# Kernel optimization log

Measured on AMD Instinct MI355X. Metric: run time of the kernel, lower is better.

Reference implementation:

```python
import jax, jax.numpy as jnp
import numpy as np

B, L, N_IN, NUM_CLASS = 2, 256, 128, 1
INIT_STD = 0.01


def setup_inputs() -> dict:
    key = jax.random.key(0)
    kx, ky, kz, kw = jax.random.split(key, 4)
    x = jax.random.normal(kx, (B, L, N_IN), dtype=jnp.float32)
    y = jax.random.normal(ky, (B, L, N_IN), dtype=jnp.float32)
    z = jax.random.normal(kz, (B, L, N_IN), dtype=jnp.float32)
    # weight: [n_in + bias_x, n_in, n_in + bias_y, num_class], init ~ N(0, init_std)
    weight = jax.random.normal(kw, (N_IN + 1, N_IN, N_IN + 1, NUM_CLASS), dtype=jnp.float32) * INIT_STD
    return {"x": x, "y": y, "z": z, "weight": weight}


def reference(x, y, z, weight):
    # bias_x / bias_y: append a ones column to x and y
    xb = jnp.concatenate([x, jnp.ones_like(x[..., :1])], axis=-1)  # [B, L, n_in+1]
    yb = jnp.concatenate([y, jnp.ones_like(y[..., :1])], axis=-1)  # [B, L, n_in+1]
    # 4-way triaffine contraction -> [B, Lx, Ly, Lz, r]
    s = jnp.einsum('bxi,bzk,ikjr,byj->bxyzr', xb, z, weight, yb, optimize=True)
    # num_class == 1: squeeze last dim (original returns before applying scale)
    return s[..., 0]
```

## Files before the change

### kernel.cpp

```cpp
#include <hip/hip_runtime.h>


typedef __bf16 bf16x8 __attribute__((ext_vector_type(8)));
typedef short short4_t __attribute__((ext_vector_type(4)));
typedef float f32x4 __attribute__((ext_vector_type(4)));
typedef unsigned short ushort4_t __attribute__((ext_vector_type(4)));

#define LL 256
#define NI 128
#define NFLATP 17408
#define KJ_STRIDE 136
#define XB_STRIDE 132
#define P_STRIDE 132

__device__ __forceinline__ unsigned short f2bf(float f) {
    unsigned u = __builtin_bit_cast(unsigned, f);
    u += 0x7FFFu + ((u >> 16) & 1u);
    return (unsigned short)(u >> 16);
}
__device__ __forceinline__ float bf2f(unsigned short h) {
    return __builtin_bit_cast(float, (unsigned)h << 16);
}

__global__ __launch_bounds__(512) void stage1f_kernel(const float* __restrict__ W,
                                                      const float* __restrict__ x,
                                                      const float* __restrict__ y,
                                                      const float* __restrict__ z,
                                                      unsigned short* __restrict__ yzbf,
                                                      unsigned short* __restrict__ A2g) {
    const int blk = blockIdx.x, tid = threadIdx.x;

    if (blk >= 272) {
        int t = (blk - 272) * 512 + tid;
        int base = t * 4;
        int which = base >> 16;
        int local = base & 65535;
        const float* s = which ? z : y;
        float4 v = *(const float4*)(s + local);
        ushort4_t o;
        o[0] = f2bf(v.x); o[1] = f2bf(v.y); o[2] = f2bf(v.z); o[3] = f2bf(v.w);
        *(ushort4_t*)(yzbf + base) = o;
        return;
    }

    const int bxg = blk & 1;
    const int nb  = blk >> 1;

    __shared__ unsigned short T[128 * KJ_STRIDE];
    __shared__ unsigned short XB[256 * XB_STRIDE];

    {
        const int nl = tid & 127;
        const int ig = tid >> 7;
        const int np = nb * 128 + nl;
        const int k  = np / KJ_STRIDE;
        const int j  = np - k * KJ_STRIDE;
        const bool jok = (j <= 128);
        const float* Wkj = W + (size_t)k * 129 + j;
        float wreg[33];
#pragma unroll
        for (int r = 0; r < 33; ++r) {
            int i = ig + r * 4;
            wreg[r] = (i <= 128 && jok) ? Wkj[(size_t)i * 16512] : 0.f;
        }
#pragma unroll
        for (int r = 0; r < 33; ++r) {
            int i = ig + r * 4;
            if (i <= 128) T[nl * KJ_STRIDE + i] = f2bf(wreg[r]);
        }
    }

    {
        const float* xsrc = x + (size_t)bxg * 256 * NI;
#pragma unroll 4
        for (int c = 0; c < 16; ++c) {
            int idx = c * 512 + tid;
            float4 v = *(const float4*)(xsrc + (size_t)idx * 4);
            int fid = idx * 4;
            int row = fid >> 7, col = fid & 127;
            ushort4_t o;
            o[0] = f2bf(v.x); o[1] = f2bf(v.y); o[2] = f2bf(v.z); o[3] = f2bf(v.w);
            *(ushort4_t*)&XB[row * XB_STRIDE + col] = o;
        }
    }
    __syncthreads();

    const int wv = tid >> 6, lane = tid & 63;
    const int l15 = lane & 15, h = lane >> 4;
    const int nsub = wv & 3;
    const int bxh  = wv >> 2;
    const int nloc = nsub * 32;
    const int nglob = nb * 128 + nloc;
    const int bx0 = bxg * 256 + bxh * 128;

    bf16x8 af[2][4];
#pragma unroll
    for (int nt = 0; nt < 2; ++nt)
#pragma unroll
        for (int is = 0; is < 4; ++is)
            af[nt][is] = *(const bf16x8*)&T[(nloc + nt * 16 + l15) * KJ_STRIDE + is * 32 + 8 * h];

    f32x4 acc[2][8];
#pragma unroll
    for (int nt = 0; nt < 2; ++nt) {
        f32x4 binit;
#pragma unroll
        for (int r = 0; r < 4; ++r)
            binit[r] = bf2f(T[(nloc + nt * 16 + 4 * h + r) * KJ_STRIDE + 128]);
#pragma unroll
        for (int ct = 0; ct < 8; ++ct) acc[nt][ct] = binit;
    }

#pragma unroll
    for (int is = 0; is < 4; ++is)
#pragma unroll
        for (int ct = 0; ct < 8; ++ct) {
            bf16x8 xf = *(const bf16x8*)&XB[(bxh * 128 + ct * 16 + l15) * XB_STRIDE + is * 32 + 8 * h];
            acc[0][ct] = __builtin_amdgcn_mfma_f32_16x16x32_bf16(af[0][is], xf, acc[0][ct], 0, 0, 0);
            acc[1][ct] = __builtin_amdgcn_mfma_f32_16x16x32_bf16(af[1][is], xf, acc[1][ct], 0, 0, 0);
        }

#pragma unroll
    for (int nt = 0; nt < 2; ++nt)
#pragma unroll
        for (int ct = 0; ct < 8; ++ct) {
            ushort4_t o;
#pragma unroll
            for (int r = 0; r < 4; ++r) o[r] = f2bf(acc[nt][ct][r]);
            *(ushort4_t*)(A2g + (size_t)(bx0 + ct * 16 + l15) * NFLATP + nglob + nt * 16 + 4 * h) = o;
        }
}

__global__ __launch_bounds__(512, 4) void stage2_kernel(const unsigned short* __restrict__ ybf,
                                                        const unsigned short* __restrict__ zbf,
                                                        const unsigned short* __restrict__ A2g,
                                                        float* __restrict__ out) {
    const int bx  = blockIdx.x;
    const int b   = bx >> 8;
    const int tid = threadIdx.x;
    const int wv = tid >> 6, lane = tid & 63;
    const int l15 = lane & 15, h = lane >> 4;

    __shared__ __align__(16) unsigned short SH[LL * P_STRIDE];

    {
        const float4* src = (const float4*)(A2g + (size_t)bx * NFLATP);
        float4* dst = (float4*)SH;
        for (int t = tid; t < NFLATP / 8; t += 512) dst[t] = src[t];
    }
    __syncthreads();

    const unsigned short* yb = ybf + b * LL * NI;
    const unsigned short* zb = zbf + b * LL * NI;
    const int y0 = wv * 32;

    f32x4 accP[8][2];
#pragma unroll
    for (int kt = 0; kt < 8; ++kt)
#pragma unroll
        for (int r = 0; r < 4; ++r) {
            float bias = bf2f(SH[(kt * 16 + 4 * h + r) * KJ_STRIDE + 128]);
            accP[kt][0][r] = bias; accP[kt][1][r] = bias;
        }
#pragma unroll
    for (int js = 0; js < 4; ++js) {
        bf16x8 yf[2];
#pragma unroll
        for (int yt = 0; yt < 2; ++yt)
            yf[yt] = *(const bf16x8*)(yb + (y0 + yt * 16 + l15) * NI + js * 32 + 8 * h);
#pragma unroll
        for (int kt = 0; kt < 8; ++kt) {
            bf16x8 af = *(const bf16x8*)&SH[(kt * 16 + l15) * KJ_STRIDE + js * 32 + 8 * h];
            accP[kt][0] = __builtin_amdgcn_mfma_f32_16x16x32_bf16(af, yf[0], accP[kt][0], 0, 0, 0);
            accP[kt][1] = __builtin_amdgcn_mfma_f32_16x16x32_bf16(af, yf[1], accP[kt][1], 0, 0, 0);
        }
    }
    __syncthreads();

#pragma unroll
    for (int kt = 0; kt < 8; ++kt)
#pragma unroll
        for (int yt = 0; yt < 2; ++yt) {
            unsigned lo = (unsigned)f2bf(accP[kt][yt][0]) | ((unsigned)f2bf(accP[kt][yt][1]) << 16);
            unsigned hi = (unsigned)f2bf(accP[kt][yt][2]) | ((unsigned)f2bf(accP[kt][yt][3]) << 16);
            uint2 v; v.x = lo; v.y = hi;
            *(uint2*)&SH[(y0 + yt * 16 + l15) * P_STRIDE + kt * 16 + 4 * h] = v;
        }

    const int zg = wv & 3, yh = wv >> 2;
    const int z0 = zg * 64;
    short4_t zf[4][8];
#pragma unroll
    for (int zt = 0; zt < 4; ++zt)
#pragma unroll
        for (int kt = 0; kt < 8; ++kt)
            zf[zt][kt] = *(const short4_t*)(zb + (z0 + zt * 16 + l15) * NI + kt * 16 + 4 * h);

    __syncthreads();

    float* outb = out + (size_t)bx * (LL * LL);
#pragma unroll 1
    for (int yti = 0; yti < 8; ++yti) {
        const int yy = yh * 128 + yti * 16 + l15;
        f32x4 acc2[4];
#pragma unroll
        for (int zt = 0; zt < 4; ++zt) { acc2[zt][0] = 0.f; acc2[zt][1] = 0.f; acc2[zt][2] = 0.f; acc2[zt][3] = 0.f; }
#pragma unroll
        for (int kt = 0; kt < 8; ++kt) {
            short4_t pB = *(const short4_t*)&SH[yy * P_STRIDE + kt * 16 + 4 * h];
#pragma unroll
            for (int zt = 0; zt < 4; ++zt)
                acc2[zt] = __builtin_amdgcn_mfma_f32_16x16x16bf16_1k(zf[zt][kt], pB, acc2[zt], 0, 0, 0);
        }
#pragma unroll
        for (int zt = 0; zt < 4; ++zt)
            *(f32x4*)(outb + (size_t)yy * LL + z0 + zt * 16 + 4 * h) = acc2[zt];
    }
}

extern "C" void kernel_launch(void* const* d_in, const int* in_sizes, int n_in,
                              void* d_out, int out_size, void* d_ws, size_t ws_size,
                              hipStream_t stream) {
    const float* x = (const float*)d_in[0];
    const float* y = (const float*)d_in[1];
    const float* z = (const float*)d_in[2];
    const float* W = (const float*)d_in[3];
    float* out = (float*)d_out;

    unsigned short* yzbf = (unsigned short*)d_ws;
    unsigned short* A2g  = yzbf + 131072;

    stage1f_kernel<<<336, 512, 0, stream>>>(W, x, y, z, yzbf, A2g);
    stage2_kernel<<<512, 512, 0, stream>>>(yzbf, yzbf + 65536, A2g, out);
}
```

Before: 67.45 us.

## Fuse both stages into one persistent kernel with a global atomic barrier

Merges the weight-projection stage and the per-row output stage into a single launch of 512 blocks. A grid-wide atomic counter barrier separates the phases, with the counter cleared by a memset on each call. The first stage is restructured so each wave owns 16 weight rows and reads x directly from global memory, converting it to bf16 on the fly instead of staging it through shared memory. This removes one kernel launch and its gap, but adds a spin barrier that requires all blocks to be co-resident, plus an extra memset and redundant x loads per block.

```diff
diff --git a/kernel.cpp b/kernel.cpp
--- a/kernel.cpp
+++ b/kernel.cpp
@@ -2,6 +2,7 @@
 
 
 typedef __bf16 bf16x8 __attribute__((ext_vector_type(8)));
+typedef unsigned short ushort8_t __attribute__((ext_vector_type(8)));
 typedef short short4_t __attribute__((ext_vector_type(4)));
 typedef float f32x4 __attribute__((ext_vector_type(4)));
 typedef unsigned short ushort4_t __attribute__((ext_vector_type(4)));
@@ -10,8 +11,8 @@
 #define NI 128
 #define NFLATP 17408
 #define KJ_STRIDE 136
-#define XB_STRIDE 132
 #define P_STRIDE 132
+#define NBLK 512
 
 __device__ __forceinline__ unsigned short f2bf(float f) {
     unsigned u = __builtin_bit_cast(unsigned, f);
@@ -22,15 +23,84 @@
     return __builtin_bit_cast(float, (unsigned)h << 16);
 }
 
-__global__ __launch_bounds__(512) void stage1f_kernel(const float* __restrict__ W,
-                                                      const float* __restrict__ x,
-                                                      const float* __restrict__ y,
-                                                      const float* __restrict__ z,
-                                                      unsigned short* __restrict__ yzbf,
-                                                      unsigned short* __restrict__ A2g) {
+__global__ __launch_bounds__(512, 4) void fused_kernel(const float* __restrict__ W,
+                                                       const float* __restrict__ x,
+                                                       const float* __restrict__ y,
+                                                       const float* __restrict__ z,
+                                                       unsigned short* __restrict__ yzbf,
+                                                       unsigned short* __restrict__ A2g,
+                                                       float* __restrict__ out,
+                                                       unsigned* bar) {
     const int blk = blockIdx.x, tid = threadIdx.x;
-
-    if (blk >= 272) {
+    __shared__ __align__(16) unsigned short SH[LL * P_STRIDE];
+
+    const int wv = tid >> 6, lane = tid & 63;
+    const int l15 = lane & 15, h = lane >> 4;
+
+    if (blk < 272) {
+        {
+            const int nl = tid & 127, ig = tid >> 7;
+            const int np = (blk >> 1) * 128 + nl;
+            const int k  = np / KJ_STRIDE;
+            const int j  = np - k * KJ_STRIDE;
+            const bool jok = (j <= 128);
+            const float* Wkj = W + (size_t)k * 129 + j;
+            float wreg[33];
+#pragma unroll
+            for (int r = 0; r < 33; ++r) {
+                int i = ig + r * 4;
+                wreg[r] = (i <= 128 && jok) ? Wkj[(size_t)i * 16512] : 0.f;
+            }
+#pragma unroll
+            for (int r = 0; r < 33; ++r) {
+                int i = ig + r * 4;
+                if (i <= 128) SH[nl * KJ_STRIDE + i] = f2bf(wreg[r]);
+            }
+        }
+        __syncthreads();
+
+        const int bxg = blk & 1;
+        const int nb  = blk >> 1;
+        const int nloc  = wv * 16;
+        const int nglob = nb * 128 + nloc;
+
+        bf16x8 af[4];
+#pragma unroll
+        for (int is = 0; is < 4; ++is)
+            af[is] = *(const bf16x8*)&SH[(nloc + l15) * KJ_STRIDE + is * 32 + 8 * h];
+        f32x4 binit;
+#pragma unroll
+        for (int r = 0; r < 4; ++r)
+            binit[r] = bf2f(SH[(nloc + 4 * h + r) * KJ_STRIDE + 128]);
+
+#pragma unroll 1
+        for (int p = 0; p < 4; ++p) {
+            const int bx0 = bxg * 256 + p * 64;
+            f32x4 acc[4];
+#pragma unroll
+            for (int ct = 0; ct < 4; ++ct) acc[ct] = binit;
+#pragma unroll
+            for (int is = 0; is < 4; ++is)
+#pragma unroll
+                for (int ct = 0; ct < 4; ++ct) {
+                    const float* xs = x + (size_t)(bx0 + ct * 16 + l15) * NI + is * 32 + 8 * h;
+                    float4 a = *(const float4*)xs;
+                    float4 b = *(const float4*)(xs + 4);
+                    ushort8_t u;
+                    u[0] = f2bf(a.x); u[1] = f2bf(a.y); u[2] = f2bf(a.z); u[3] = f2bf(a.w);
+                    u[4] = f2bf(b.x); u[5] = f2bf(b.y); u[6] = f2bf(b.z); u[7] = f2bf(b.w);
+                    bf16x8 xf = __builtin_bit_cast(bf16x8, u);
+                    acc[ct] = __builtin_amdgcn_mfma_f32_16x16x32_bf16(af[is], xf, acc[ct], 0, 0, 0);
+                }
+#pragma unroll
+            for (int ct = 0; ct < 4; ++ct) {
+                ushort4_t o;
+#pragma unroll
+                for (int r = 0; r < 4; ++r) o[r] = f2bf(acc[ct][r]);
+                *(ushort4_t*)(A2g + (size_t)(bx0 + ct * 16 + l15) * NFLATP + nglob + 4 * h) = o;
+            }
+        }
+    } else if (blk < 336) {
         int t = (blk - 272) * 512 + tid;
         int base = t * 4;
         int which = base >> 16;
@@ -40,108 +110,20 @@
         ushort4_t o;
         o[0] = f2bf(v.x); o[1] = f2bf(v.y); o[2] = f2bf(v.z); o[3] = f2bf(v.w);
         *(ushort4_t*)(yzbf + base) = o;
-        return;
-    }
-
-    const int bxg = blk & 1;
-    const int nb  = blk >> 1;
-
-    __shared__ unsigned short T[128 * KJ_STRIDE];
-    __shared__ unsigned short XB[256 * XB_STRIDE];
-
-    {
-        const int nl = tid & 127;
-        const int ig = tid >> 7;
-        const int np = nb * 128 + nl;
-        const int k  = np / KJ_STRIDE;
-        const int j  = np - k * KJ_STRIDE;
-        const bool jok = (j <= 128);
-        const float* Wkj = W + (size_t)k * 129 + j;
-        float wreg[33];
-#pragma unroll
-        for (int r = 0; r < 33; ++r) {
-            int i = ig + r * 4;
-            wreg[r] = (i <= 128 && jok) ? Wkj[(size_t)i * 16512] : 0.f;
-        }
-#pragma unroll
-        for (int r = 0; r < 33; ++r) {
-            int i = ig + r * 4;
-            if (i <= 128) T[nl * KJ_STRIDE + i] = f2bf(wreg[r]);
-        }
-    }
-
-    {
-        const float* xsrc = x + (size_t)bxg * 256 * NI;
-#pragma unroll 4
-        for (int c = 0; c < 16; ++c) {
-            int idx = c * 512 + tid;
-            float4 v = *(const float4*)(xsrc + (size_t)idx * 4);
-            int fid = idx * 4;
-            int row = fid >> 7, col = fid & 127;
-            ushort4_t o;
-            o[0] = f2bf(v.x); o[1] = f2bf(v.y); o[2] = f2bf(v.z); o[3] = f2bf(v.w);
-            *(ushort4_t*)&XB[row * XB_STRIDE + col] = o;
-        }
-    }
-    __syncthreads();
-
-    const int wv = tid >> 6, lane = tid & 63;
-    const int l15 = lane & 15, h = lane >> 4;
-    const int nsub = wv & 3;
-    const int bxh  = wv >> 2;
-    const int nloc = nsub * 32;
-    const int nglob = nb * 128 + nloc;
-    const int bx0 = bxg * 256 + bxh * 128;
-
-    bf16x8 af[2][4];
-#pragma unroll
-    for (int nt = 0; nt < 2; ++nt)
-#pragma unroll
-        for (int is = 0; is < 4; ++is)
-            af[nt][is] = *(const bf16x8*)&T[(nloc + nt * 16 + l15) * KJ_STRIDE + is * 32 + 8 * h];
-
-    f32x4 acc[2][8];
-#pragma unroll
-    for (int nt = 0; nt < 2; ++nt) {
-        f32x4 binit;
-#pragma unroll
-        for (int r = 0; r < 4; ++r)
-            binit[r] = bf2f(T[(nloc + nt * 16 + 4 * h + r) * KJ_STRIDE + 128]);
-#pragma unroll
-        for (int ct = 0; ct < 8; ++ct) acc[nt][ct] = binit;
-    }
-
-#pragma unroll
-    for (int is = 0; is < 4; ++is)
-#pragma unroll
-        for (int ct = 0; ct < 8; ++ct) {
-            bf16x8 xf = *(const bf16x8*)&XB[(bxh * 128 + ct * 16 + l15) * XB_STRIDE + is * 32 + 8 * h];
-            acc[0][ct] = __builtin_amdgcn_mfma_f32_16x16x32_bf16(af[0][is], xf, acc[0][ct], 0, 0, 0);
-            acc[1][ct] = __builtin_amdgcn_mfma_f32_16x16x32_bf16(af[1][is], xf, acc[1][ct], 0, 0, 0);
-        }
-
-#pragma unroll
-    for (int nt = 0; nt < 2; ++nt)
-#pragma unroll
-        for (int ct = 0; ct < 8; ++ct) {
-            ushort4_t o;
-#pragma unroll
-            for (int r = 0; r < 4; ++r) o[r] = f2bf(acc[nt][ct][r]);
-            *(ushort4_t*)(A2g + (size_t)(bx0 + ct * 16 + l15) * NFLATP + nglob + nt * 16 + 4 * h) = o;
-        }
-}
-
-__global__ __launch_bounds__(512, 4) void stage2_kernel(const unsigned short* __restrict__ ybf,
-                                                        const unsigned short* __restrict__ zbf,
-                                                        const unsigned short* __restrict__ A2g,
-                                                        float* __restrict__ out) {
-    const int bx  = blockIdx.x;
-    const int b   = bx >> 8;
-    const int tid = threadIdx.x;
-    const int wv = tid >> 6, lane = tid & 63;
-    const int l15 = lane & 15, h = lane >> 4;
-
-    __shared__ __align__(16) unsigned short SH[LL * P_STRIDE];
+    }
+
+    __syncthreads();
+    if (tid == 0) {
+        __threadfence();
+        atomicAdd(bar, 1u);
+        while (__hip_atomic_load(bar, __ATOMIC_ACQUIRE, __HIP_MEMORY_SCOPE_AGENT) < NBLK)
+            __builtin_amdgcn_s_sleep(8);
+        __threadfence();
+    }
+    __syncthreads();
+
+    const int bx = blk;
+    const int b  = bx >> 8;
 
     {
         const float4* src = (const float4*)(A2g + (size_t)bx * NFLATP);
@@ -150,8 +132,8 @@
     }
     __syncthreads();
 
-    const unsigned short* yb = ybf + b * LL * NI;
-    const unsigned short* zb = zbf + b * LL * NI;
+    const unsigned short* yb = yzbf + b * LL * NI;
+    const unsigned short* zb = yzbf + 65536 + b * LL * NI;
     const int y0 = wv * 32;
 
     f32x4 accP[8][2];
@@ -170,9 +152,9 @@
             yf[yt] = *(const bf16x8*)(yb + (y0 + yt * 16 + l15) * NI + js * 32 + 8 * h);
 #pragma unroll
         for (int kt = 0; kt < 8; ++kt) {
-            bf16x8 af = *(const bf16x8*)&SH[(kt * 16 + l15) * KJ_STRIDE + js * 32 + 8 * h];
-            accP[kt][0] = __builtin_amdgcn_mfma_f32_16x16x32_bf16(af, yf[0], accP[kt][0], 0, 0, 0);
-            accP[kt][1] = __builtin_amdgcn_mfma_f32_16x16x32_bf16(af, yf[1], accP[kt][1], 0, 0, 0);
+            bf16x8 af2 = *(const bf16x8*)&SH[(kt * 16 + l15) * KJ_STRIDE + js * 32 + 8 * h];
+            accP[kt][0] = __builtin_amdgcn_mfma_f32_16x16x32_bf16(af2, yf[0], accP[kt][0], 0, 0, 0);
+            accP[kt][1] = __builtin_amdgcn_mfma_f32_16x16x32_bf16(af2, yf[1], accP[kt][1], 0, 0, 0);
         }
     }
     __syncthreads();
@@ -227,9 +209,10 @@
     const float* W = (const float*)d_in[3];
     float* out = (float*)d_out;
 
-    unsigned short* yzbf = (unsigned short*)d_ws;
+    unsigned* bar = (unsigned*)d_ws;
+    unsigned short* yzbf = (unsigned short*)((char*)d_ws + 256);
     unsigned short* A2g  = yzbf + 131072;
 
-    stage1f_kernel<<<336, 512, 0, stream>>>(W, x, y, z, yzbf, A2g);
-    stage2_kernel<<<512, 512, 0, stream>>>(yzbf, yzbf + 65536, A2g, out);
-}
+    hipMemsetAsync(bar, 0, 256, stream);
+    fused_kernel<<<NBLK, 512, 0, stream>>>(W, x, y, z, yzbf, A2g, out, bar);
+}
```

New measurement: 260.0 us. 285% more time.
